# Kernel optimization log

Measured on AMD Instinct MI355X. Metric: run time of the kernel, lower is better.

Reference implementation:

```python
import jax, jax.numpy as jnp
import numpy as np

B, S, D = 2, 2048, 1024   # batch, seq, in_shape
H, E = 16, 64             # num_heads, out_shape (per-head dim)

def setup_inputs() -> dict:
    key = jax.random.key(0)
    ks = jax.random.split(key, 5)
    x = jax.random.normal(ks[0], (B, S, D), dtype=jnp.float32)
    Wq = jax.random.normal(ks[1], (H, D, E), dtype=jnp.float32) * 0.02
    Wk = jax.random.normal(ks[2], (H, D, E), dtype=jnp.float32) * 0.02
    Wv = jax.random.normal(ks[3], (H, D, E), dtype=jnp.float32) * 0.02
    W = jax.random.normal(ks[4], (H * E, E), dtype=jnp.float32) * 0.02
    return {"x": x, "Wq": Wq, "Wk": Wk, "Wv": Wv, "W": W}

def reference(x, Wq, Wk, Wv, W):
    # Per-head projections (stacked over heads): [B,H,S,E]
    q = jnp.einsum("bsd,hde->bhse", x, Wq)
    k = jnp.einsum("bsd,hde->bhse", x, Wk)
    v = jnp.einsum("bsd,hde->bhse", x, Wv)
    scale = 1.0 / jnp.sqrt(jnp.float32(E))
    # Full causal scores [B,H,S,S] with -inf above diagonal (as in original)
    scores = jnp.einsum("bhse,bhte->bhst", q, k) * scale
    causal = jnp.tril(jnp.ones((S, S), dtype=bool))
    scores = jnp.where(causal, scores, -jnp.inf)
    attn = jax.nn.softmax(scores, axis=-1)
    ctx = jnp.einsum("bhst,bhte->bhse", attn, v)          # [B,H,S,E]
    # concat heads along last dim (head-major order matches tf.concat over list)
    ctx = jnp.transpose(ctx, (0, 2, 1, 3)).reshape(B, S, H * E)
    return ctx @ W                                         # [B,S,E]
```

## Files before the change

kernel.cpp:

```cpp
#include <hip/hip_runtime.h>
#include <hip/hip_bf16.h>
#include <cstdint>
#include <cstddef>

#define BB 2
#define SS 2048
#define DD 1024
#define HH 16
#define EE 64

typedef short bf16x8 __attribute__((ext_vector_type(8)));
typedef short s4 __attribute__((ext_vector_type(4)));
typedef float f32x4 __attribute__((ext_vector_type(4)));
typedef float float4v __attribute__((ext_vector_type(4)));
typedef unsigned int u32x2 __attribute__((ext_vector_type(2)));
typedef unsigned int u32x4 __attribute__((ext_vector_type(4)));

#define GLDS(gp, lp) __builtin_amdgcn_global_load_lds( \
    (const __attribute__((address_space(1))) void*)(gp), \
    (__attribute__((address_space(3))) void*)(lp), 16, 0, 0)

static __device__ __forceinline__ short f2bf(float f) {
    union { float f; uint32_t u; } v; v.f = f;
    uint32_t r = (v.u + 0x7fffu + ((v.u >> 16) & 1u)) >> 16;
    return (short)r;
}

static __device__ __forceinline__ uint32_t cvtpk(float a, float b) {
    uint32_t r;
    asm("v_cvt_pk_bf16_f32 %0, %1, %2" : "=v"(r) : "v"(a), "v"(b));
    return r;
}

__global__ __launch_bounds__(256) void prep_kernel(const float* __restrict__ x,
                                                   const float* __restrict__ Wq,
                                                   const float* __restrict__ Wk,
                                                   const float* __restrict__ Wv,
                                                   const float* __restrict__ W,
                                                   short* __restrict__ xb,
                                                   short* __restrict__ wt,
                                                   short* __restrict__ wot) {
    __shared__ float tile[64][65];
    int blk = blockIdx.x;
    int t = threadIdx.x;
    if (blk < 4096) {
        int i = blk * 256 + t;
        float4v v = ((const float4v*)x)[i];
        s4 o; o[0] = f2bf(v[0]); o[1] = f2bf(v[1]); o[2] = f2bf(v[2]); o[3] = f2bf(v[3]);
        ((s4*)xb)[i] = o;
        return;
    }
    int idx = blk - 4096;
    const float* src;
    short* d;
    int R, r0;
    if (idx < 768) {
        int bx = idx & 15, by = idx >> 4;
        int which = by >> 4, mtx = by & 15;
        src = ((which == 0) ? Wq : (which == 1) ? Wk : Wv) + (size_t)mtx * DD * 64;
        d = wt + (size_t)which * HH * EE * DD + (size_t)mtx * DD * 64;
        R = DD; r0 = bx * 64;
    } else {
        int bx = idx - 768;
        src = W; d = wot; R = HH * EE; r0 = bx * 64;
    }
#pragma unroll
    for (int i = 0; i < 16; ++i) {
        int id2 = t + i * 256;
        int r = id2 >> 6, c = id2 & 63;
        tile[r][c] = src[(size_t)(r0 + r) * 64 + c];
    }
    __syncthreads();
#pragma unroll
    for (int i = 0; i < 16; ++i) {
        int id2 = t + i * 256;
        int e = id2 >> 6, dd2 = id2 & 63;
        d[(size_t)e * R + r0 + dd2] = f2bf(tile[dd2][e]);
    }
}

__global__ __launch_bounds__(256, 3) void qkv_gemm(const short* __restrict__ A,
                                                   const short* __restrict__ Bt,
                                                   short* __restrict__ Qo,
                                                   short* __restrict__ Ko,
                                                   short* __restrict__ Vto) {
    __shared__ __align__(16) short As3[3][64 * 64];
    __shared__ __align__(16) short Bs3[3][64 * 64];
    int tid = threadIdx.x;
    int wv = tid >> 6, lane = tid & 63;
    int m = lane & 15, g = lane >> 4;
    int wr = wv >> 1, wc = wv & 1;

    int xcd = blockIdx.x & 7, idx = blockIdx.x >> 3;
    int mb = (xcd & 3) * 8 + (idx & 7);
    int nb = (xcd >> 2) * 12 + (idx >> 3);
    int rowBase = mb * 128, colBase0 = nb * 128;

    int src_row[2], src_kcol[2];
#pragma unroll
    for (int j = 0; j < 2; ++j) {
        int si = j * 256 + tid;
        int sr = si >> 3, sp = si & 7;
        int sl = sp ^ (sr & 7);
        src_row[j] = 2 * sr + (sl >> 2);
        src_kcol[j] = (sl & 3) * 8;
    }
    const short* aP0 = A + (size_t)(rowBase + src_row[0]) * DD + src_kcol[0];
    const short* aP1 = A + (size_t)(rowBase + src_row[1]) * DD + src_kcol[1];
    const short* bP0 = Bt + (size_t)(colBase0 + src_row[0]) * DD + src_kcol[0];
    const short* bP1 = Bt + (size_t)(colBase0 + src_row[1]) * DD + src_kcol[1];
    int dst0 = (wv * 64) * 8;
    int dst1 = (256 + wv * 64) * 8;

    f32x4 acc[4][4];
#pragma unroll
    for (int i = 0; i < 4; ++i)
#pragma unroll
        for (int j = 0; j < 4; ++j) acc[i][j] = {0, 0, 0, 0};

    int rdoff = ((m & 1) * 64 + g * 16) ^ (((m >> 1) & 7) << 4);
    int mh = m >> 1;

    auto STAGE = [&](int buf, int kt) {
        short* ab = &As3[buf][0];
        short* bb = &Bs3[buf][0];
        GLDS(aP0 + kt, ab + dst0);
        GLDS(aP1 + kt, ab + dst1);
        GLDS(bP0 + kt, bb + dst0);
        GLDS(bP1 + kt, bb + dst1);
    };

    auto COMPUTE = [&](int buf) {
        bf16x8 af[4], bfr[4];
#pragma unroll
        for (int mi = 0; mi < 4; ++mi)
            af[mi] = *(const bf16x8*)((const char*)&As3[buf][(wr * 32 + mi * 8 + mh) * 64] + rdoff);
#pragma unroll
        for (int ni = 0; ni < 4; ++ni)
            bfr[ni] = *(const bf16x8*)((const char*)&Bs3[buf][(wc * 32 + ni * 8 + mh) * 64] + rdoff);
        asm volatile("s_waitcnt lgkmcnt(0)\ns_barrier" ::: "memory");
        __builtin_amdgcn_s_setprio(1);
#pragma unroll
        for (int mi = 0; mi < 4; ++mi)
#pragma unroll
            for (int ni = 0; ni < 4; ++ni)
                acc[mi][ni] = __builtin_amdgcn_mfma_f32_16x16x32_bf16(af[mi], bfr[ni], acc[mi][ni], 0, 0, 0);
        __builtin_amdgcn_s_setprio(0);
    };

    STAGE(0, 0);
    STAGE(1, 32);
    for (int t = 0; t < 30; ++t) {
        STAGE((t + 2) % 3, (t + 2) * 32);
        asm volatile("s_waitcnt vmcnt(8)\ns_barrier" ::: "memory");
        COMPUTE(t % 3);
    }
    asm volatile("s_waitcnt vmcnt(4)\ns_barrier" ::: "memory");
    COMPUTE(0);
    asm volatile("s_waitcnt vmcnt(0)\ns_barrier" ::: "memory");
    COMPUTE(1);

    int colw = colBase0 + wc * 64;
    int mtx = colw >> 10;
    int h = (colw >> 6) & 15;
    int rb = rowBase + wr * 64;

    if (mtx == 0) {
        const float qs = 0.125f * 1.44269504089f;
#pragma unroll
        for (int mi = 0; mi < 4; ++mi)
#pragma unroll
            for (int ni = 0; ni < 4; ++ni)
#pragma unroll
                for (int r = 0; r < 4; ++r) {
                    int row = rb + mi * 16 + g * 4 + r;
                    int b = row >> 11, s = row & 2047;
                    Qo[((size_t)(b * HH + h) * SS + s) * EE + ni * 16 + m] = f2bf(acc[mi][ni][r] * qs);
                }
    } else if (mtx == 1) {
#pragma unroll
        for (int mi = 0; mi < 4; ++mi)
#pragma unroll
            for (int ni = 0; ni < 4; ++ni)
#pragma unroll
                for (int r = 0; r < 4; ++r) {
                    int row = rb + mi * 16 + g * 4 + r;
                    int b = row >> 11, s = row & 2047;
                    Ko[((size_t)(b * HH + h) * SS + s) * EE + ni * 16 + m] = f2bf(acc[mi][ni][r]);
                }
    } else {
#pragma unroll
        for (int mi = 0; mi < 4; ++mi)
#pragma unroll
            for (int ni = 0; ni < 4; ++ni) {
                int row0 = rb + mi * 16 + g * 4;
                int b = row0 >> 11, s = row0 & 2047;
                s4 o; o[0] = f2bf(acc[mi][ni][0]); o[1] = f2bf(acc[mi][ni][1]);
                o[2] = f2bf(acc[mi][ni][2]); o[3] = f2bf(acc[mi][ni][3]);
                *(s4*)&Vto[((size_t)(b * HH + h) * EE + ni * 16 + m) * SS + s] = o;
            }
    }
}

__global__ __launch_bounds__(256, 5) void attn_kernel(const short* __restrict__ Q,
                                                      const short* __restrict__ K,
                                                      const short* __restrict__ Vt,
                                                      short* __restrict__ ctx) {
    __shared__ __align__(16) short Ks[2][64 * 64];
    __shared__ __align__(16) short Vs[2][64 * 64];
    int tid = threadIdx.x;
    int wv = tid >> 6, lane = tid & 63;
    int m = lane & 15, g = lane >> 4;
    int xcd = blockIdx.x & 7, i = blockIdx.x >> 3;
    int bh = xcd * 4 + (i & 3);
    int qblk = 31 - (i >> 2);
    int b = bh >> 4, h = bh & 15;
    const short* Qb = Q + (size_t)bh * SS * EE;
    const short* Kb = K + (size_t)bh * SS * EE;
    const short* Vb = Vt + (size_t)bh * EE * SS;
    int qrow = qblk * 64 + wv * 16 + m;

    int srow = wv * 8 + (lane >> 3);
    int scol_s = (((lane & 7) * 16) ^ ((srow & 7) << 4)) >> 1;
    int trow = ((srow >> 4) & 1) * 32 + ((srow >> 2) & 3) * 8 + (srow & 3);

    bf16x8 qa0 = *(const bf16x8*)(Qb + (size_t)qrow * EE + g * 8);
    bf16x8 qa1 = *(const bf16x8*)(Qb + (size_t)qrow * EE + 32 + g * 8);

    int sw = (m & 7) << 4;
    int c0 = (g * 16) ^ sw;
    int c1 = (64 + g * 16) ^ sw;

    float lsum = 0.f;
    f32x4 o[4];
#pragma unroll
    for (int n = 0; n < 4; ++n) { o[n][0] = 0.f; o[n][1] = 0.f; o[n][2] = 0.f; o[n][3] = 0.f; }

    auto STAGE = [&](int nb, int t0) {
        short* kd = &Ks[0][0] + nb * 4096 + wv * 512;
        short* vd = &Vs[0][0] + nb * 4096 + wv * 512;
        const short* ksrc = Kb + (size_t)(t0 + trow) * EE + scol_s;
        const short* vsrc = Vb + (size_t)srow * SS + t0 + scol_s;
        GLDS(ksrc, kd);
        GLDS(ksrc + 4 * EE, kd + 2048);
        GLDS(vsrc, vd);
        GLDS(vsrc + (size_t)32 * SS, vd + 2048);
    };

    int ntile = qblk + 1;
    STAGE(0, 0);
    __syncthreads();

    for (int tt = 0; tt < ntile; ++tt) {
        if (tt + 1 < ntile) STAGE((tt + 1) & 1, (tt + 1) * 64);
        int t0 = tt * 64;
        const short* Ksb = &Ks[0][0] + (tt & 1) * 4096;
        const short* Vsb = &Vs[0][0] + (tt & 1) * 4096;

        f32x4 sc[4] = {{-16.f,-16.f,-16.f,-16.f},{-16.f,-16.f,-16.f,-16.f},
                       {-16.f,-16.f,-16.f,-16.f},{-16.f,-16.f,-16.f,-16.f}};
#pragma unroll
        for (int n = 0; n < 4; ++n) {
            const char* krow = (const char*)(Ksb + (n * 16 + m) * 64);
            bf16x8 kb0 = *(const bf16x8*)(krow + c0);
            sc[n] = __builtin_amdgcn_mfma_f32_16x16x32_bf16(kb0, qa0, sc[n], 0, 0, 0);
            bf16x8 kb1 = *(const bf16x8*)(krow + c1);
            sc[n] = __builtin_amdgcn_mfma_f32_16x16x32_bf16(kb1, qa1, sc[n], 0, 0, 0);
        }

        if (tt == qblk) {
#pragma unroll
            for (int n = 0; n < 4; ++n)
#pragma unroll
                for (int r = 0; r < 4; ++r) {
                    int t = t0 + 32 * (n & 1) + 8 * g + 4 * (n >> 1) + r;
                    if (t > qrow) sc[n][r] = -INFINITY;
                }
        }

#pragma unroll
        for (int n = 0; n < 4; ++n) {
            sc[n][0] = exp2f(sc[n][0]);
            sc[n][1] = exp2f(sc[n][1]);
            sc[n][2] = exp2f(sc[n][2]);
            sc[n][3] = exp2f(sc[n][3]);
            lsum += (sc[n][0] + sc[n][1]) + (sc[n][2] + sc[n][3]);
        }

#pragma unroll
        for (int ks = 0; ks < 2; ++ks) {
            union { u32x4 w; bf16x8 v; } pu;
            pu.w[0] = cvtpk(sc[ks][0], sc[ks][1]);
            pu.w[1] = cvtpk(sc[ks][2], sc[ks][3]);
            pu.w[2] = cvtpk(sc[ks + 2][0], sc[ks + 2][1]);
            pu.w[3] = cvtpk(sc[ks + 2][2], sc[ks + 2][3]);
            bf16x8 pa = pu.v;
            int cv = ks ? c1 : c0;
#pragma unroll
            for (int n = 0; n < 4; ++n) {
                const char* vrow = (const char*)(Vsb + (n * 16 + m) * 64);
                bf16x8 vb = *(const bf16x8*)(vrow + cv);
                o[n] = __builtin_amdgcn_mfma_f32_16x16x32_bf16(vb, pa, o[n], 0, 0, 0);
            }
        }

        __syncthreads();
    }

    lsum += __shfl_xor(lsum, 16, 64);
    lsum += __shfl_xor(lsum, 32, 64);
    float inv = 1.0f / lsum;
    short* cb = ctx + (size_t)(b * SS + qrow) * (HH * EE) + h * EE;
#pragma unroll
    for (int n = 0; n < 4; ++n) {
        u32x2 k0; k0[0] = cvtpk(o[n][0] * inv, o[n][1] * inv);
        k0[1] = cvtpk(o[n][2] * inv, o[n][3] * inv);
        *(u32x2*)&cb[n * 16 + g * 4] = k0;
    }
}

__global__ __launch_bounds__(256) void outproj_kernel(const short* __restrict__ ctx,
                                                      const short* __restrict__ wot,
                                                      float* __restrict__ out) {
    __shared__ float red[4][1024];
    int wv = threadIdx.x >> 6, lane = threadIdx.x & 63;
    int m = lane & 15, g = lane >> 4;
    int r0 = blockIdx.x * 16;
    const short* arow = ctx + (size_t)(r0 + m) * (HH * EE) + g * 8;
    const short* wb = wot + g * 8;
    f32x4 acc[4] = {{0,0,0,0},{0,0,0,0},{0,0,0,0},{0,0,0,0}};
    int k0 = wv * 256;
    for (int d0 = k0; d0 < k0 + 256; d0 += 32) {
        bf16x8 a = *(const bf16x8*)(arow + d0);
#pragma unroll
        for (int n = 0; n < 4; ++n) {
            bf16x8 bbf = *(const bf16x8*)(wb + (size_t)(n * 16 + m) * (HH * EE) + d0);
            acc[n] = __builtin_amdgcn_mfma_f32_16x16x32_bf16(a, bbf, acc[n], 0, 0, 0);
        }
    }
#pragma unroll
    for (int n = 0; n < 4; ++n)
#pragma unroll
        for (int r = 0; r < 4; ++r)
            red[wv][(g * 4 + r) * 64 + n * 16 + m] = acc[n][r];
    __syncthreads();
    int t = threadIdx.x;
    float4v sum = ((const float4v*)red[0])[t];
    sum += ((const float4v*)red[1])[t];
    sum += ((const float4v*)red[2])[t];
    sum += ((const float4v*)red[3])[t];
    ((float4v*)(out + (size_t)blockIdx.x * 1024))[t] = sum;
}

extern "C" void kernel_launch(void* const* d_in, const int* in_sizes, int n_in,
                              void* d_out, int out_size, void* d_ws, size_t ws_size,
                              hipStream_t stream) {
    const float* x  = (const float*)d_in[0];
    const float* Wq = (const float*)d_in[1];
    const float* Wk = (const float*)d_in[2];
    const float* Wv = (const float*)d_in[3];
    const float* W  = (const float*)d_in[4];
    float* out = (float*)d_out;

    char* w = (char*)d_ws;
    short* xb  = (short*)w;
    short* wqt = (short*)(w + ((size_t)8 << 20));
    short* wot = wqt + (size_t)3 * HH * EE * DD;
    short* Qb  = wot + (size_t)64 * 1024;
    short* Kb  = Qb + (size_t)BB * HH * SS * EE;
    short* Vtb = Kb + (size_t)BB * HH * SS * EE;
    short* ctx = Vtb + (size_t)BB * HH * SS * EE;

    prep_kernel<<<4880, 256, 0, stream>>>(x, Wq, Wk, Wv, W, xb, wqt, wot);
    qkv_gemm<<<768, 256, 0, stream>>>(xb, wqt, Qb, Kb, Vtb);
    attn_kernel<<<1024, 256, 0, stream>>>(Qb, Kb, Vtb, ctx);
    outproj_kernel<<<256, 256, 0, stream>>>(ctx, wot, out);
}
```

Before: 85.70 us.

## Use two-wave attention blocks with each wave computing 32 query rows

Attention blocks shrink from four waves to two, and each wave now handles two 16-row query tiles, so every K/V fragment read from LDS feeds twice as many MFMAs. Staging is split by role: wave 0 loads the K tile and wave 1 loads the V tile, eight global-to-LDS copies each. MFMA sections are wrapped in s_setprio to favour matrix issue. The cost is higher register pressure from doubled accumulators and fewer waves per block, which may reduce latency hiding.

```diff
diff --git a/kernel.cpp b/kernel.cpp
--- a/kernel.cpp
+++ b/kernel.cpp
@@ -202,7 +202,7 @@
     }
 }
 
-__global__ __launch_bounds__(256, 5) void attn_kernel(const short* __restrict__ Q,
+__global__ __launch_bounds__(128, 2) void attn_kernel(const short* __restrict__ Q,
                                                       const short* __restrict__ K,
                                                       const short* __restrict__ Vt,
                                                       short* __restrict__ ctx) {
@@ -218,33 +218,45 @@
     const short* Qb = Q + (size_t)bh * SS * EE;
     const short* Kb = K + (size_t)bh * SS * EE;
     const short* Vb = Vt + (size_t)bh * EE * SS;
-    int qrow = qblk * 64 + wv * 16 + m;
-
-    int srow = wv * 8 + (lane >> 3);
-    int scol_s = (((lane & 7) * 16) ^ ((srow & 7) << 4)) >> 1;
-    int trow = ((srow >> 4) & 1) * 32 + ((srow >> 2) & 3) * 8 + (srow & 3);
-
-    bf16x8 qa0 = *(const bf16x8*)(Qb + (size_t)qrow * EE + g * 8);
-    bf16x8 qa1 = *(const bf16x8*)(Qb + (size_t)qrow * EE + 32 + g * 8);
+    int qrow0 = qblk * 64 + wv * 32 + m;
+    int qrow1 = qrow0 + 16;
+
+    int u = lane >> 3;
+    int scol_s = (((lane & 7) * 16) ^ (u << 4)) >> 1;
+    int tlane = 8 * (u >> 2) + (u & 3);
+    constexpr int CJ[8] = {0, 16, 32, 48, 4, 20, 36, 52};
+
+    bf16x8 qa00 = *(const bf16x8*)(Qb + (size_t)qrow0 * EE + g * 8);
+    bf16x8 qa01 = *(const bf16x8*)(Qb + (size_t)qrow0 * EE + 32 + g * 8);
+    bf16x8 qa10 = *(const bf16x8*)(Qb + (size_t)qrow1 * EE + g * 8);
+    bf16x8 qa11 = *(const bf16x8*)(Qb + (size_t)qrow1 * EE + 32 + g * 8);
 
     int sw = (m & 7) << 4;
     int c0 = (g * 16) ^ sw;
     int c1 = (64 + g * 16) ^ sw;
 
-    float lsum = 0.f;
-    f32x4 o[4];
-#pragma unroll
-    for (int n = 0; n < 4; ++n) { o[n][0] = 0.f; o[n][1] = 0.f; o[n][2] = 0.f; o[n][3] = 0.f; }
+    float lsum0 = 0.f, lsum1 = 0.f;
+    f32x4 o0[4], o1[4];
+#pragma unroll
+    for (int n = 0; n < 4; ++n) {
+        o0[n][0] = 0.f; o0[n][1] = 0.f; o0[n][2] = 0.f; o0[n][3] = 0.f;
+        o1[n][0] = 0.f; o1[n][1] = 0.f; o1[n][2] = 0.f; o1[n][3] = 0.f;
+    }
 
     auto STAGE = [&](int nb, int t0) {
-        short* kd = &Ks[0][0] + nb * 4096 + wv * 512;
-        short* vd = &Vs[0][0] + nb * 4096 + wv * 512;
-        const short* ksrc = Kb + (size_t)(t0 + trow) * EE + scol_s;
-        const short* vsrc = Vb + (size_t)srow * SS + t0 + scol_s;
-        GLDS(ksrc, kd);
-        GLDS(ksrc + 4 * EE, kd + 2048);
-        GLDS(vsrc, vd);
-        GLDS(vsrc + (size_t)32 * SS, vd + 2048);
+        if (wv == 0) {
+            short* kd = &Ks[0][0] + nb * 4096;
+            const short* ks0 = Kb + (size_t)(t0 + tlane) * EE + scol_s;
+#pragma unroll
+            for (int j = 0; j < 8; ++j)
+                GLDS(ks0 + CJ[j] * EE, kd + j * 512);
+        } else {
+            short* vd = &Vs[0][0] + nb * 4096;
+            const short* vs0 = Vb + (size_t)u * SS + t0 + scol_s;
+#pragma unroll
+            for (int j = 0; j < 8; ++j)
+                GLDS(vs0 + (size_t)(j * 8) * SS, vd + j * 512);
+        }
     };
 
     int ntile = qblk + 1;
@@ -257,16 +269,24 @@
         const short* Ksb = &Ks[0][0] + (tt & 1) * 4096;
         const short* Vsb = &Vs[0][0] + (tt & 1) * 4096;
 
-        f32x4 sc[4] = {{-16.f,-16.f,-16.f,-16.f},{-16.f,-16.f,-16.f,-16.f},
-                       {-16.f,-16.f,-16.f,-16.f},{-16.f,-16.f,-16.f,-16.f}};
+        f32x4 s0[4], s1[4];
+#pragma unroll
+        for (int n = 0; n < 4; ++n) {
+            s0[n] = {-16.f, -16.f, -16.f, -16.f};
+            s1[n] = {-16.f, -16.f, -16.f, -16.f};
+        }
+        __builtin_amdgcn_s_setprio(1);
 #pragma unroll
         for (int n = 0; n < 4; ++n) {
             const char* krow = (const char*)(Ksb + (n * 16 + m) * 64);
             bf16x8 kb0 = *(const bf16x8*)(krow + c0);
-            sc[n] = __builtin_amdgcn_mfma_f32_16x16x32_bf16(kb0, qa0, sc[n], 0, 0, 0);
             bf16x8 kb1 = *(const bf16x8*)(krow + c1);
-            sc[n] = __builtin_amdgcn_mfma_f32_16x16x32_bf16(kb1, qa1, sc[n], 0, 0, 0);
-        }
+            s0[n] = __builtin_amdgcn_mfma_f32_16x16x32_bf16(kb0, qa00, s0[n], 0, 0, 0);
+            s0[n] = __builtin_amdgcn_mfma_f32_16x16x32_bf16(kb1, qa01, s0[n], 0, 0, 0);
+            s1[n] = __builtin_amdgcn_mfma_f32_16x16x32_bf16(kb0, qa10, s1[n], 0, 0, 0);
+            s1[n] = __builtin_amdgcn_mfma_f32_16x16x32_bf16(kb1, qa11, s1[n], 0, 0, 0);
+        }
+        __builtin_amdgcn_s_setprio(0);
 
         if (tt == qblk) {
 #pragma unroll
@@ -274,48 +294,63 @@
 #pragma unroll
                 for (int r = 0; r < 4; ++r) {
                     int t = t0 + 32 * (n & 1) + 8 * g + 4 * (n >> 1) + r;
-                    if (t > qrow) sc[n][r] = -INFINITY;
+                    if (t > qrow0) s0[n][r] = -INFINITY;
+                    if (t > qrow1) s1[n][r] = -INFINITY;
                 }
         }
 
 #pragma unroll
         for (int n = 0; n < 4; ++n) {
-            sc[n][0] = exp2f(sc[n][0]);
-            sc[n][1] = exp2f(sc[n][1]);
-            sc[n][2] = exp2f(sc[n][2]);
-            sc[n][3] = exp2f(sc[n][3]);
-            lsum += (sc[n][0] + sc[n][1]) + (sc[n][2] + sc[n][3]);
+            s0[n][0] = exp2f(s0[n][0]); s0[n][1] = exp2f(s0[n][1]);
+            s0[n][2] = exp2f(s0[n][2]); s0[n][3] = exp2f(s0[n][3]);
+            lsum0 += (s0[n][0] + s0[n][1]) + (s0[n][2] + s0[n][3]);
+            s1[n][0] = exp2f(s1[n][0]); s1[n][1] = exp2f(s1[n][1]);
+            s1[n][2] = exp2f(s1[n][2]); s1[n][3] = exp2f(s1[n][3]);
+            lsum1 += (s1[n][0] + s1[n][1]) + (s1[n][2] + s1[n][3]);
         }
 
 #pragma unroll
         for (int ks = 0; ks < 2; ++ks) {
-            union { u32x4 w; bf16x8 v; } pu;
-            pu.w[0] = cvtpk(sc[ks][0], sc[ks][1]);
-            pu.w[1] = cvtpk(sc[ks][2], sc[ks][3]);
-            pu.w[2] = cvtpk(sc[ks + 2][0], sc[ks + 2][1]);
-            pu.w[3] = cvtpk(sc[ks + 2][2], sc[ks + 2][3]);
-            bf16x8 pa = pu.v;
+            union { u32x4 w; bf16x8 v; } p0, p1;
+            p0.w[0] = cvtpk(s0[ks][0], s0[ks][1]);
+            p0.w[1] = cvtpk(s0[ks][2], s0[ks][3]);
+            p0.w[2] = cvtpk(s0[ks + 2][0], s0[ks + 2][1]);
+            p0.w[3] = cvtpk(s0[ks + 2][2], s0[ks + 2][3]);
+            p1.w[0] = cvtpk(s1[ks][0], s1[ks][1]);
+            p1.w[1] = cvtpk(s1[ks][2], s1[ks][3]);
+            p1.w[2] = cvtpk(s1[ks + 2][0], s1[ks + 2][1]);
+            p1.w[3] = cvtpk(s1[ks + 2][2], s1[ks + 2][3]);
             int cv = ks ? c1 : c0;
+            __builtin_amdgcn_s_setprio(1);
 #pragma unroll
             for (int n = 0; n < 4; ++n) {
                 const char* vrow = (const char*)(Vsb + (n * 16 + m) * 64);
                 bf16x8 vb = *(const bf16x8*)(vrow + cv);
-                o[n] = __builtin_amdgcn_mfma_f32_16x16x32_bf16(vb, pa, o[n], 0, 0, 0);
+                o0[n] = __builtin_amdgcn_mfma_f32_16x16x32_bf16(vb, p0.v, o0[n], 0, 0, 0);
+                o1[n] = __builtin_amdgcn_mfma_f32_16x16x32_bf16(vb, p1.v, o1[n], 0, 0, 0);
             }
+            __builtin_amdgcn_s_setprio(0);
         }
 
         __syncthreads();
     }
 
-    lsum += __shfl_xor(lsum, 16, 64);
-    lsum += __shfl_xor(lsum, 32, 64);
-    float inv = 1.0f / lsum;
-    short* cb = ctx + (size_t)(b * SS + qrow) * (HH * EE) + h * EE;
+    lsum0 += __shfl_xor(lsum0, 16, 64);
+    lsum0 += __shfl_xor(lsum0, 32, 64);
+    lsum1 += __shfl_xor(lsum1, 16, 64);
+    lsum1 += __shfl_xor(lsum1, 32, 64);
+    float inv0 = 1.0f / lsum0;
+    float inv1 = 1.0f / lsum1;
+    short* cb0 = ctx + (size_t)(b * SS + qrow0) * (HH * EE) + h * EE;
+    short* cb1 = ctx + (size_t)(b * SS + qrow1) * (HH * EE) + h * EE;
 #pragma unroll
     for (int n = 0; n < 4; ++n) {
-        u32x2 k0; k0[0] = cvtpk(o[n][0] * inv, o[n][1] * inv);
-        k0[1] = cvtpk(o[n][2] * inv, o[n][3] * inv);
-        *(u32x2*)&cb[n * 16 + g * 4] = k0;
+        u32x2 k0; k0[0] = cvtpk(o0[n][0] * inv0, o0[n][1] * inv0);
+        k0[1] = cvtpk(o0[n][2] * inv0, o0[n][3] * inv0);
+        *(u32x2*)&cb0[n * 16 + g * 4] = k0;
+        u32x2 k1; k1[0] = cvtpk(o1[n][0] * inv1, o1[n][1] * inv1);
+        k1[1] = cvtpk(o1[n][2] * inv1, o1[n][3] * inv1);
+        *(u32x2*)&cb1[n * 16 + g * 4] = k1;
     }
 }
 
@@ -373,6 +408,6 @@
 
     prep_kernel<<<4880, 256, 0, stream>>>(x, Wq, Wk, Wv, W, xb, wqt, wot);
     qkv_gemm<<<768, 256, 0, stream>>>(xb, wqt, Qb, Kb, Vtb);
-    attn_kernel<<<1024, 256, 0, stream>>>(Qb, Kb, Vtb, ctx);
+    attn_kernel<<<1024, 128, 0, stream>>>(Qb, Kb, Vtb, ctx);
     outproj_kernel<<<256, 256, 0, stream>>>(ctx, wot, out);
 }
```

New measurement: 101.8 us. 1.19x slower.

## Split attention KV tiles across two wave groups with LDS reduction

Applied to the files above, without the earlier changes.

The attention block grows to 512 threads. The two groups of four waves take alternating 64-key tiles (even and odd) for the same 64 query rows, keeping separate partial output and row-sum accumulators. These partials are merged through LDS at the end, and then the first group writes the normalized output. The aim is more parallelism per query block and less serial latency on the long causal rows. The cost is that half the waves sit idle on each tile while the other half computes, plus an extra barrier and reduction, and launch bounds with 8 waves per EU may tighten registers.

```diff
diff --git a/kernel.cpp b/kernel.cpp
--- a/kernel.cpp
+++ b/kernel.cpp
@@ -202,7 +202,7 @@
     }
 }
 
-__global__ __launch_bounds__(256, 5) void attn_kernel(const short* __restrict__ Q,
+__global__ __launch_bounds__(512, 8) void attn_kernel(const short* __restrict__ Q,
                                                       const short* __restrict__ K,
                                                       const short* __restrict__ Vt,
                                                       short* __restrict__ ctx) {
@@ -211,6 +211,7 @@
     int tid = threadIdx.x;
     int wv = tid >> 6, lane = tid & 63;
     int m = lane & 15, g = lane >> 4;
+    int par = wv >> 2;
     int xcd = blockIdx.x & 7, i = blockIdx.x >> 3;
     int bh = xcd * 4 + (i & 3);
     int qblk = 31 - (i >> 2);
@@ -218,11 +219,11 @@
     const short* Qb = Q + (size_t)bh * SS * EE;
     const short* Kb = K + (size_t)bh * SS * EE;
     const short* Vb = Vt + (size_t)bh * EE * SS;
-    int qrow = qblk * 64 + wv * 16 + m;
-
-    int srow = wv * 8 + (lane >> 3);
-    int scol_s = (((lane & 7) * 16) ^ ((srow & 7) << 4)) >> 1;
-    int trow = ((srow >> 4) & 1) * 32 + ((srow >> 2) & 3) * 8 + (srow & 3);
+    int qrow = qblk * 64 + (wv & 3) * 16 + m;
+
+    int sr = tid >> 3, sp = tid & 7;
+    int scol_s = ((sp * 16) ^ ((sr & 7) << 4)) >> 1;
+    int trow = ((sr >> 4) & 1) * 32 + ((sr >> 2) & 3) * 8 + (sr >> 5) * 4 + (sr & 3);
 
     bf16x8 qa0 = *(const bf16x8*)(Qb + (size_t)qrow * EE + g * 8);
     bf16x8 qa1 = *(const bf16x8*)(Qb + (size_t)qrow * EE + 32 + g * 8);
@@ -237,14 +238,10 @@
     for (int n = 0; n < 4; ++n) { o[n][0] = 0.f; o[n][1] = 0.f; o[n][2] = 0.f; o[n][3] = 0.f; }
 
     auto STAGE = [&](int nb, int t0) {
-        short* kd = &Ks[0][0] + nb * 4096 + wv * 512;
-        short* vd = &Vs[0][0] + nb * 4096 + wv * 512;
-        const short* ksrc = Kb + (size_t)(t0 + trow) * EE + scol_s;
-        const short* vsrc = Vb + (size_t)srow * SS + t0 + scol_s;
-        GLDS(ksrc, kd);
-        GLDS(ksrc + 4 * EE, kd + 2048);
-        GLDS(vsrc, vd);
-        GLDS(vsrc + (size_t)32 * SS, vd + 2048);
+        short* kd = &Ks[nb][0] + wv * 512;
+        short* vd = &Vs[nb][0] + wv * 512;
+        GLDS(Kb + (size_t)(t0 + trow) * EE + scol_s, kd);
+        GLDS(Vb + (size_t)sr * SS + t0 + scol_s, vd);
     };
 
     int ntile = qblk + 1;
@@ -253,59 +250,77 @@
 
     for (int tt = 0; tt < ntile; ++tt) {
         if (tt + 1 < ntile) STAGE((tt + 1) & 1, (tt + 1) * 64);
-        int t0 = tt * 64;
-        const short* Ksb = &Ks[0][0] + (tt & 1) * 4096;
-        const short* Vsb = &Vs[0][0] + (tt & 1) * 4096;
-
-        f32x4 sc[4] = {{-16.f,-16.f,-16.f,-16.f},{-16.f,-16.f,-16.f,-16.f},
-                       {-16.f,-16.f,-16.f,-16.f},{-16.f,-16.f,-16.f,-16.f}};
-#pragma unroll
-        for (int n = 0; n < 4; ++n) {
-            const char* krow = (const char*)(Ksb + (n * 16 + m) * 64);
-            bf16x8 kb0 = *(const bf16x8*)(krow + c0);
-            sc[n] = __builtin_amdgcn_mfma_f32_16x16x32_bf16(kb0, qa0, sc[n], 0, 0, 0);
-            bf16x8 kb1 = *(const bf16x8*)(krow + c1);
-            sc[n] = __builtin_amdgcn_mfma_f32_16x16x32_bf16(kb1, qa1, sc[n], 0, 0, 0);
+
+        if ((tt & 1) == par) {
+            int t0 = tt * 64;
+            const short* Ksb = &Ks[tt & 1][0];
+            const short* Vsb = &Vs[tt & 1][0];
+
+            f32x4 sc[4] = {{-16.f,-16.f,-16.f,-16.f},{-16.f,-16.f,-16.f,-16.f},
+                           {-16.f,-16.f,-16.f,-16.f},{-16.f,-16.f,-16.f,-16.f}};
+#pragma unroll
+            for (int n = 0; n < 4; ++n) {
+                const char* krow = (const char*)(Ksb + (n * 16 + m) * 64);
+                bf16x8 kb0 = *(const bf16x8*)(krow + c0);
+                sc[n] = __builtin_amdgcn_mfma_f32_16x16x32_bf16(kb0, qa0, sc[n], 0, 0, 0);
+                bf16x8 kb1 = *(const bf16x8*)(krow + c1);
+                sc[n] = __builtin_amdgcn_mfma_f32_16x16x32_bf16(kb1, qa1, sc[n], 0, 0, 0);
+            }
+
+            if (tt == qblk) {
+#pragma unroll
+                for (int n = 0; n < 4; ++n)
+#pragma unroll
+                    for (int r = 0; r < 4; ++r) {
+                        int t = t0 + 32 * (n & 1) + 8 * g + 4 * (n >> 1) + r;
+                        if (t > qrow) sc[n][r] = -INFINITY;
+                    }
+            }
+
+#pragma unroll
+            for (int n = 0; n < 4; ++n) {
+                sc[n][0] = exp2f(sc[n][0]);
+                sc[n][1] = exp2f(sc[n][1]);
+                sc[n][2] = exp2f(sc[n][2]);
+                sc[n][3] = exp2f(sc[n][3]);
+                lsum += (sc[n][0] + sc[n][1]) + (sc[n][2] + sc[n][3]);
+            }
+
+#pragma unroll
+            for (int ks = 0; ks < 2; ++ks) {
+                union { u32x4 w; bf16x8 v; } pu;
+                pu.w[0] = cvtpk(sc[ks][0], sc[ks][1]);
+                pu.w[1] = cvtpk(sc[ks][2], sc[ks][3]);
+                pu.w[2] = cvtpk(sc[ks + 2][0], sc[ks + 2][1]);
+                pu.w[3] = cvtpk(sc[ks + 2][2], sc[ks + 2][3]);
+                bf16x8 pa = pu.v;
+                int cv = ks ? c1 : c0;
+#pragma unroll
+                for (int n = 0; n < 4; ++n) {
+                    const char* vrow = (const char*)(Vsb + (n * 16 + m) * 64);
+                    bf16x8 vb = *(const bf16x8*)(vrow + cv);
+                    o[n] = __builtin_amdgcn_mfma_f32_16x16x32_bf16(vb, pa, o[n], 0, 0, 0);
+                }
+            }
         }
 
-        if (tt == qblk) {
-#pragma unroll
-            for (int n = 0; n < 4; ++n)
-#pragma unroll
-                for (int r = 0; r < 4; ++r) {
-                    int t = t0 + 32 * (n & 1) + 8 * g + 4 * (n >> 1) + r;
-                    if (t > qrow) sc[n][r] = -INFINITY;
-                }
-        }
-
-#pragma unroll
-        for (int n = 0; n < 4; ++n) {
-            sc[n][0] = exp2f(sc[n][0]);
-            sc[n][1] = exp2f(sc[n][1]);
-            sc[n][2] = exp2f(sc[n][2]);
-            sc[n][3] = exp2f(sc[n][3]);
-            lsum += (sc[n][0] + sc[n][1]) + (sc[n][2] + sc[n][3]);
-        }
-
-#pragma unroll
-        for (int ks = 0; ks < 2; ++ks) {
-            union { u32x4 w; bf16x8 v; } pu;
-            pu.w[0] = cvtpk(sc[ks][0], sc[ks][1]);
-            pu.w[1] = cvtpk(sc[ks][2], sc[ks][3]);
-            pu.w[2] = cvtpk(sc[ks + 2][0], sc[ks + 2][1]);
-            pu.w[3] = cvtpk(sc[ks + 2][2], sc[ks + 2][3]);
-            bf16x8 pa = pu.v;
-            int cv = ks ? c1 : c0;
-#pragma unroll
-            for (int n = 0; n < 4; ++n) {
-                const char* vrow = (const char*)(Vsb + (n * 16 + m) * 64);
-                bf16x8 vb = *(const bf16x8*)(vrow + cv);
-                o[n] = __builtin_amdgcn_mfma_f32_16x16x32_bf16(vb, pa, o[n], 0, 0, 0);
-            }
-        }
-
         __syncthreads();
     }
+
+    float* xo = (float*)&Ks[0][0];
+    float* xl = (float*)&Vs[0][0];
+    if (par == 1) {
+        float4v* dst = (float4v*)(xo + (wv - 4) * 1024 + lane * 16);
+#pragma unroll
+        for (int n = 0; n < 4; ++n) dst[n] = o[n];
+        xl[(wv - 4) * 64 + lane] = lsum;
+    }
+    __syncthreads();
+    if (par == 1) return;
+    const float4v* src = (const float4v*)(xo + wv * 1024 + lane * 16);
+#pragma unroll
+    for (int n = 0; n < 4; ++n) o[n] += src[n];
+    lsum += xl[wv * 64 + lane];
 
     lsum += __shfl_xor(lsum, 16, 64);
     lsum += __shfl_xor(lsum, 32, 64);
@@ -373,6 +388,6 @@
 
     prep_kernel<<<4880, 256, 0, stream>>>(x, Wq, Wk, Wv, W, xb, wqt, wot);
     qkv_gemm<<<768, 256, 0, stream>>>(xb, wqt, Qb, Kb, Vtb);
-    attn_kernel<<<1024, 256, 0, stream>>>(Qb, Kb, Vtb, ctx);
+    attn_kernel<<<1024, 512, 0, stream>>>(Qb, Kb, Vtb, ctx);
     outproj_kernel<<<256, 256, 0, stream>>>(ctx, wot, out);
 }
```

Result: slower. 92.01 us (+7.4%).
